# Optimization experiments

Hardware: AMD Instinct MI355X
Metric: run time of the kernel (lower is better)

## Reference

```python
import jax, jax.numpy as jnp
import numpy as np

PRE_NMS_TOP_N = 1024
POST_NMS_TOP_N = 256
NMS_THRESH = 0.7
MIN_SIZE = 4.0
SCORE_THRESH = 0.1
BASE_SIZE = 1024.0
SCALE = 0.25            # feature stride = 1/SCALE = 4
IMG_H, IMG_W = 1024.0, 1024.0
NEG_INF = -1e30
CAP = 8                 # max vertices of 4-gon intersect 4-gon


def setup_inputs() -> dict:
    key = jax.random.key(0)
    k1, k2 = jax.random.split(key)
    N, A, H, W = 2, 1, 256, 256
    objectness = jax.random.normal(k1, (N, A, H, W), dtype=jnp.float32)
    box_regression = jax.random.uniform(k2, (N, A * 5, H, W), dtype=jnp.float32) * 0.05
    return {"objectness": objectness, "box_regression": box_regression}


def eastbox2rbox(reg, H, W):
    # reg: (H*W, 5) -> rotated boxes (H*W, 5) in xywha (angle in degrees)
    jy, jx = jnp.meshgrid(jnp.arange(H, dtype=reg.dtype), jnp.arange(W, dtype=reg.dtype), indexing="ij")
    cx0 = (jx / SCALE).reshape(-1)
    cy0 = (jy / SCALE).reshape(-1)
    t = reg[:, 0] * BASE_SIZE
    r = reg[:, 1] * BASE_SIZE
    b = reg[:, 2] * BASE_SIZE
    l = reg[:, 3] * BASE_SIZE
    ang = (reg[:, 4] - 0.5) * 90.0
    w = l + r
    h = t + b
    xc = cx0 + 0.5 * (r - l)
    yc = cy0 + 0.5 * (b - t)
    return jnp.stack([xc, yc, w, h, ang], axis=-1)


def rbox_corners(box):
    # box: (5,) xywha -> (4,2) CCW corners
    th = box[4] * (jnp.pi / 180.0)
    c, s = jnp.cos(th), jnp.sin(th)
    dx = jnp.array([-0.5, 0.5, 0.5, -0.5], box.dtype) * box[2]
    dy = jnp.array([-0.5, -0.5, 0.5, 0.5], box.dtype) * box[3]
    return jnp.stack([box[0] + dx * c - dy * s, box[1] + dx * s + dy * c], axis=-1)


def clip_halfplane(poly, n, p1, p2):
    # Sutherland-Hodgman clip of a convex polygon (CAP,2) with n valid verts
    # against the half-plane left of directed edge p1->p2.
    M = poly.shape[0]
    idx = jnp.arange(M)
    valid = idx < n
    nxt = poly[jnp.where(idx + 1 < n, idx + 1, 0)]
    e = p2 - p1
    d_cur = e[0] * (poly[:, 1] - p1[1]) - e[1] * (poly[:, 0] - p1[0])
    d_nxt = e[0] * (nxt[:, 1] - p1[1]) - e[1] * (nxt[:, 0] - p1[0])
    in_cur = d_cur >= 0.0
    in_nxt = d_nxt >= 0.0
    denom = d_cur - d_nxt
    safe = jnp.where(jnp.abs(denom) > 1e-9, denom, 1.0)
    t = d_cur / safe
    inter = poly + t[:, None] * (nxt - poly)
    emit_cur = in_cur & valid
    emit_int = (in_cur != in_nxt) & valid
    pts = jnp.stack([poly, inter], axis=1).reshape(2 * M, 2)
    flags = jnp.stack([emit_cur, emit_int], axis=1).reshape(2 * M)
    pos = jnp.where(flags, jnp.cumsum(flags) - 1, M)  # M = dropped
    out = jnp.zeros((M, 2), poly.dtype).at[pos].set(jnp.where(flags[:, None], pts, 0.0), mode="drop")
    return out, jnp.sum(flags)


def intersect_area(pa, pb):
    # area of convex intersection of two 4-gons (each (4,2), CCW)
    poly = jnp.zeros((CAP, 2), pa.dtype).at[:4].set(pa)
    n = jnp.asarray(4, jnp.int32)
    for k in range(4):
        poly, n = clip_halfplane(poly, n, pb[k], pb[(k + 1) % 4])
    idx = jnp.arange(CAP)
    valid = idx < n
    nxt = poly[jnp.where(idx + 1 < n, idx + 1, 0)]
    cr = poly[:, 0] * nxt[:, 1] - nxt[:, 0] * poly[:, 1]
    area = 0.5 * jnp.abs(jnp.sum(jnp.where(valid, cr, 0.0)))
    return jnp.where(n >= 3, area, 0.0)


def riou(a, b):
    inter = intersect_area(rbox_corners(a), rbox_corners(b))
    union = a[2] * a[3] + b[2] * b[3] - inter
    return inter / jnp.maximum(union, 1e-9)


def greedy_nms(iou_mat, valid, thresh):
    K = valid.shape[0]
    ar = jnp.arange(K)

    def body(i, state):
        keep, sup = state
        is_keep = valid[i] & jnp.logical_not(sup[i])
        keep = keep.at[i].set(is_keep)
        sup = sup | (is_keep & (iou_mat[i] > thresh) & (ar > i))
        return keep, sup

    keep, _ = jax.lax.fori_loop(0, K, body, (jnp.zeros(K, bool), jnp.zeros(K, bool)))
    return keep


def process_image(obj, reg):
    A, H, W = obj.shape
    scores = obj.transpose(1, 2, 0).reshape(-1)       # (H*W*A,)
    reg5 = reg[:5].transpose(1, 2, 0).reshape(-1, 5)  # (H*W, 5)
    rboxes = eastbox2rbox(reg5, H, W)
    top_scores, top_idx = jax.lax.top_k(scores, PRE_NMS_TOP_N)
    boxes = rboxes[top_idx]
    valid = top_scores > SCORE_THRESH                 # eval-mode score thresh (masked, not dropped)
    # clip_to_image: clamp rotated-box centers into the image
    boxes = boxes.at[:, 0].set(jnp.clip(boxes[:, 0], 0.0, IMG_W - 1.0))
    boxes = boxes.at[:, 1].set(jnp.clip(boxes[:, 1], 0.0, IMG_H - 1.0))
    # remove_small_boxes
    valid = valid & (boxes[:, 2] >= MIN_SIZE) & (boxes[:, 3] >= MIN_SIZE)
    # full rotated IoU matrix, row-by-row to bound memory
    iou_mat = jax.lax.map(lambda a: jax.vmap(lambda b: riou(a, b))(boxes), boxes)
    keep = greedy_nms(iou_mat, valid, NMS_THRESH)
    sel = jnp.where(keep, top_scores, NEG_INF)
    fin_scores, fin_idx = jax.lax.top_k(sel, POST_NMS_TOP_N)
    fin_boxes = boxes[fin_idx]
    fin_valid = keep[fin_idx]
    out = jnp.concatenate([fin_boxes, fin_scores[:, None]], axis=-1)  # (post, 6) = xywha + score
    return jnp.where(fin_valid[:, None], out, 0.0)


def reference(objectness, box_regression):
    return jax.vmap(process_image)(objectness, box_regression)
```

## Files before the change

### kernel.cpp

```cpp
#include <hip/hip_runtime.h>
#include <hip/hip_bf16.h>

#define N_IMG 2
#define HW 65536
#define PRE 1024
#define POST 256
#define NBIN 4096
#define SORTN 4096
#define NMS_THR 0.7f
#define SCORE_T 0.1f
#define MIN_SZ 4.0f
#define TRIPAIRS 523776
#define TRITOTAL (2 * TRIPAIRS)

__device__ __forceinline__ unsigned int fkey(float f) {
    unsigned int u = __float_as_uint(f);
    return u ^ ((u & 0x80000000u) ? 0xFFFFFFFFu : 0x80000000u);
}
__device__ __forceinline__ float unfkey(unsigned int k) {
    unsigned int u = (k & 0x80000000u) ? (k ^ 0x80000000u) : ~k;
    return __uint_as_float(u);
}
__device__ __forceinline__ unsigned long long readlane64(unsigned long long v, int l) {
    unsigned int lo = (unsigned int)__builtin_amdgcn_readlane((int)(unsigned int)v, l);
    unsigned int hi = (unsigned int)__builtin_amdgcn_readlane((int)(unsigned int)(v >> 32), l);
    return ((unsigned long long)hi << 32) | (unsigned long long)lo;
}

__global__ __launch_bounds__(1024) void k_front(const float* __restrict__ obj,
                                                unsigned int* phist,
                                                unsigned long long* masks,
                                                unsigned int* cnts) {
    __shared__ unsigned int lh[NBIN];
    int img = blockIdx.x >> 3;
    int seg = blockIdx.x & 7;
    for (int i = threadIdx.x; i < NBIN; i += 1024) lh[i] = 0u;
    {
        unsigned long long* mz = masks + (size_t)blockIdx.x * 2048;
        mz[threadIdx.x] = 0ULL;
        mz[threadIdx.x + 1024] = 0ULL;
    }
    if (blockIdx.x == 0 && threadIdx.x < 8) cnts[threadIdx.x] = 0u;
    __syncthreads();
    const float4* o4 = (const float4*)(obj + (size_t)img * HW);
    int base = seg * 2048;
#pragma unroll
    for (int k = 0; k < 2; ++k) {
        float4 v = o4[base + threadIdx.x + k * 1024];
        atomicAdd(&lh[fkey(v.x) >> 20], 1u);
        atomicAdd(&lh[fkey(v.y) >> 20], 1u);
        atomicAdd(&lh[fkey(v.z) >> 20], 1u);
        atomicAdd(&lh[fkey(v.w) >> 20], 1u);
    }
    __syncthreads();
    unsigned int* ph = phist + (size_t)blockIdx.x * NBIN;
    for (int i = threadIdx.x; i < NBIN; i += 1024) ph[i] = lh[i];
}

__global__ void k_findbin(const unsigned int* __restrict__ phist, unsigned int* selB) {
    __shared__ unsigned int lh[NBIN];
    __shared__ unsigned int chunk[256];
    int img = blockIdx.x;
    int t = threadIdx.x;
    for (int c = 0; c < 16; ++c) {
        int b = c * 256 + t;
        unsigned int v = 0;
#pragma unroll
        for (int q = 0; q < 8; ++q) v += phist[(size_t)(img * 8 + q) * NBIN + b];
        lh[b] = v;
    }
    __syncthreads();
    unsigned int s = 0;
    for (int k = 0; k < 16; ++k) s += lh[t * 16 + k];
    chunk[t] = s;
    __syncthreads();
    if (t == 0) {
        unsigned int run = 0;
        int c;
        for (c = 255; c >= 0; --c) {
            if (run + chunk[c] >= PRE) break;
            run += chunk[c];
        }
        unsigned int B = 0;
        for (int b = c * 16 + 15; b >= c * 16; --b) {
            if (run + lh[b] >= PRE) { B = (unsigned int)b; break; }
            run += lh[b];
        }
        selB[img] = B;
    }
}

__global__ __launch_bounds__(256) void k_compact(const float* __restrict__ obj,
                                                 const unsigned int* __restrict__ selB,
                                                 unsigned int* cnts, unsigned long long* cbuf) {
    __shared__ unsigned long long lbuf[1024];
    __shared__ unsigned int lcnt, lbase;
    int t = blockIdx.x * 256 + threadIdx.x;
    const float4* o4 = (const float4*)obj;
#pragma unroll
    for (int k = 0; k < 2; ++k) {
        if (threadIdx.x == 0) lcnt = 0;
        __syncthreads();
        int p = t + k * 16384;
        int img = p >> 14;
        unsigned int B = selB[img];
        float4 v = o4[p];
        float vs[4] = {v.x, v.y, v.z, v.w};
#pragma unroll
        for (int c = 0; c < 4; ++c) {
            unsigned int key = fkey(vs[c]);
            if ((key >> 20) >= B) {
                unsigned int i = (unsigned int)((p & 16383) * 4 + c);
                unsigned int pos = atomicAdd(&lcnt, 1u);
                lbuf[pos] = ((unsigned long long)key << 32) |
                            (unsigned long long)(0xFFFFFFFFu - i);
            }
        }
        __syncthreads();
        if (threadIdx.x == 0) lbase = atomicAdd(&cnts[img], lcnt);
        __syncthreads();
        unsigned int n = lcnt, base = lbase;
        for (unsigned int q = threadIdx.x; q < n; q += 256) {
            unsigned int gp = base + q;
            if (gp < SORTN) cbuf[img * SORTN + gp] = lbuf[q];
        }
        __syncthreads();
    }
}

__device__ __forceinline__ void decode_one(unsigned long long cv, int img,
                                           const float* __restrict__ boxreg,
                                           float* boxes, float* corn, float4* circ,
                                           unsigned int* varr, float* tscr, int r) {
    int g = img * PRE + r;
    unsigned int key = (unsigned int)(cv >> 32);
    unsigned int idx = (0xFFFFFFFFu - (unsigned int)(cv & 0xFFFFFFFFULL)) & 0xFFFFu;
    float sc = unfkey(key);
    int h = (int)(idx >> 8);
    int w = (int)(idx & 255u);
    const float* rg = boxreg + (size_t)img * 5 * HW;
    float t_ = rg[0 * HW + idx] * 1024.0f;
    float rr = rg[1 * HW + idx] * 1024.0f;
    float bb = rg[2 * HW + idx] * 1024.0f;
    float ll = rg[3 * HW + idx] * 1024.0f;
    float ang = (rg[4 * HW + idx] - 0.5f) * 90.0f;
    float wd = ll + rr;
    float ht = t_ + bb;
    float xc = (float)w * 4.0f + 0.5f * (rr - ll);
    float yc = (float)h * 4.0f + 0.5f * (bb - t_);
    xc = fminf(fmaxf(xc, 0.0f), 1023.0f);
    yc = fminf(fmaxf(yc, 0.0f), 1023.0f);
    bool valid = (sc > SCORE_T) && (wd >= MIN_SZ) && (ht >= MIN_SZ);

    float* bx = boxes + (size_t)g * 5;
    bx[0] = xc; bx[1] = yc; bx[2] = wd; bx[3] = ht; bx[4] = ang;
    tscr[g] = sc;
    varr[g] = valid ? 1u : 0u;

    float th = ang * (float)(3.14159265358979323846 / 180.0);
    float c = cosf(th), s = sinf(th);
    const float dxs[4] = {-0.5f, 0.5f, 0.5f, -0.5f};
    const float dys[4] = {-0.5f, -0.5f, 0.5f, 0.5f};
    float* cr = corn + (size_t)g * 8;
#pragma unroll
    for (int k = 0; k < 4; ++k) {
        float dx = dxs[k] * wd, dy = dys[k] * ht;
        cr[2 * k]     = xc + dx * c - dy * s;
        cr[2 * k + 1] = yc + dx * s + dy * c;
    }
    circ[g] = make_float4(xc, yc, 0.5f * sqrtf(wd * wd + ht * ht) + 0.01f, wd * ht);
}

__global__ __launch_bounds__(256) void k_rankdec(const unsigned int* __restrict__ cnts,
                                                 const unsigned long long* __restrict__ cbuf,
                                                 const float* __restrict__ boxreg,
                                                 float* boxes, float* corn, float4* circ,
                                                 unsigned int* varr, float* tscr) {
    __shared__ unsigned long long keys[SORTN];
    int img = blockIdx.x >> 4;
    int slice = blockIdx.x & 15;
    unsigned int M = cnts[img]; if (M > SORTN) M = SORTN;
    for (unsigned int i = threadIdx.x; i < M; i += 256) keys[i] = cbuf[img * SORTN + i];
    __syncthreads();
    unsigned int cid = (unsigned int)slice * 256 + threadIdx.x;
    if (cid >= M) return;
    unsigned long long cv = keys[cid];
    unsigned int r = 0;
    for (unsigned int j = 0; j < M; ++j) r += (keys[j] > cv) ? 1u : 0u;
    if (r < PRE) decode_one(cv, img, boxreg, boxes, corn, circ, varr, tscr, (int)r);
}

__global__ __launch_bounds__(256) void k_pairclip(const float4* __restrict__ circ,
                                                  const float* __restrict__ corn,
                                                  unsigned long long* masks) {
    __shared__ struct {
        float SPX[8][256], SPY[8][256], SQX[8][256], SQY[8][256];
        unsigned int plist[1280];
    } e;
    __shared__ unsigned int pcnt;
    int tid = threadIdx.x;
    if (tid == 0) pcnt = 0;
    __syncthreads();
    int t0 = blockIdx.x * 256 + tid;
    for (int k = 0; k < 8; ++k) {
        int s = t0 + k * 131072;
        if (s < TRITOTAL) {
            int img = (s >= TRIPAIRS) ? 1 : 0;
            int p = s - img * TRIPAIRS;
            int r = (int)((sqrtf((float)(8 * p + 1)) - 1.0f) * 0.5f);
            while ((r * (r + 1)) / 2 > p) --r;
            while (((r + 1) * (r + 2)) / 2 <= p) ++r;
            int i = p - (r * (r + 1)) / 2;
            int j = r + 1;
            float4 a = circ[img * PRE + i];
            float4 b = circ[img * PRE + j];
            float dx = b.x - a.x, dy = b.y - a.y, rr = a.z + b.z;
            if (dx * dx + dy * dy <= rr * rr)
                e.plist[atomicAdd(&pcnt, 1u)] =
                    ((unsigned int)img << 20) | ((unsigned int)i << 10) | (unsigned int)j;
        }
        __syncthreads();
        unsigned int n = pcnt;
        if (n >= 1024 || k == 7) {
            for (unsigned int q = tid; q < n; q += 256) {
                unsigned int pr = e.plist[q];
                int im = (int)(pr >> 20);
                int bi = (int)((pr >> 10) & 1023);
                int bj = (int)(pr & 1023);
                int ra = im * PRE + bi, rb = im * PRE + bj;
                const float4* ca = (const float4*)(corn + (size_t)ra * 8);
                float4 a0 = ca[0], a1 = ca[1];
                const float4* cb = (const float4*)(corn + (size_t)rb * 8);
                float4 b0 = cb[0], b1 = cb[1];
                float cbx[4] = {b0.x, b0.z, b1.x, b1.z};
                float cby[4] = {b0.y, b0.w, b1.y, b1.w};
                e.SPX[0][tid] = a0.x; e.SPY[0][tid] = a0.y;
                e.SPX[1][tid] = a0.z; e.SPY[1][tid] = a0.w;
                e.SPX[2][tid] = a1.x; e.SPY[2][tid] = a1.y;
                e.SPX[3][tid] = a1.z; e.SPY[3][tid] = a1.w;
                int n2 = 4;
#pragma unroll
                for (int ed = 0; ed < 4; ++ed) {
                    float (*PX)[256] = (ed & 1) ? e.SQX : e.SPX;
                    float (*PY)[256] = (ed & 1) ? e.SQY : e.SPY;
                    float (*QX)[256] = (ed & 1) ? e.SPX : e.SQX;
                    float (*QY)[256] = (ed & 1) ? e.SPY : e.SQY;
                    float p1x = cbx[ed], p1y = cby[ed];
                    int e2 = (ed + 1) & 3;
                    float ex = cbx[e2] - p1x, ey = cby[e2] - p1y;
                    int m = 0;
                    for (int kk = 0; kk < n2; ++kk) {
                        int kn = (kk + 1 < n2) ? kk + 1 : 0;
                        float cx_ = PX[kk][tid], cy_ = PY[kk][tid];
                        float nx_ = PX[kn][tid], ny_ = PY[kn][tid];
                        float dc = ex * (cy_ - p1y) - ey * (cx_ - p1x);
                        float dn = ex * (ny_ - p1y) - ey * (nx_ - p1x);
                        bool ic = dc >= 0.0f;
                        bool inx = dn >= 0.0f;
                        if (ic && m < 8) { QX[m][tid] = cx_; QY[m][tid] = cy_; ++m; }
                        if ((ic != inx) && m < 8) {
                            float den = dc - dn;
                            float safe = (fabsf(den) > 1e-9f) ? den : 1.0f;
                            float tt = dc / safe;
                            QX[m][tid] = cx_ + tt * (nx_ - cx_);
                            QY[m][tid] = cy_ + tt * (ny_ - cy_);
                            ++m;
                        }
                    }
                    n2 = m;
                }
                float inter = 0.0f;
                if (n2 >= 3) {
                    float sa = 0.0f;
                    for (int kk = 0; kk < n2; ++kk) {
                        int kn = (kk + 1 < n2) ? kk + 1 : 0;
                        sa += e.SPX[kk][tid] * e.SPY[kn][tid] - e.SPX[kn][tid] * e.SPY[kk][tid];
                    }
                    inter = 0.5f * fabsf(sa);
                }
                float uni = circ[ra].w + circ[rb].w - inter;
                float iou = inter / fmaxf(uni, 1e-9f);
                if (iou > NMS_THR)
                    atomicOr(&masks[(size_t)ra * 16 + (bj >> 6)], 1ULL << (bj & 63));
            }
            __syncthreads();
            if (tid == 0) pcnt = 0;
            __syncthreads();
        }
    }
}

__global__ __launch_bounds__(1024) void k_nms_out(const unsigned long long* __restrict__ masks,
                                                  const unsigned int* __restrict__ varr,
                                                  const float* __restrict__ boxes,
                                                  const float* __restrict__ tscr,
                                                  float* __restrict__ out) {
    __shared__ unsigned long long lm[PRE * 16];
    __shared__ unsigned long long vmw_s[16];
    __shared__ unsigned short keptIdx[POST];
    __shared__ int sTotal;
    int img = blockIdx.x;
    int t = threadIdx.x;
    const unsigned long long* mbase = masks + (size_t)img * PRE * 16;
    {
        const ulonglong2* src = (const ulonglong2*)mbase;
        ulonglong2* dst = (ulonglong2*)lm;
#pragma unroll
        for (int k = 0; k < 8; ++k) dst[t + k * 1024] = src[t + k * 1024];
    }
    {
        unsigned long long bal = __ballot(varr[img * PRE + t] != 0u);
        if ((t & 63) == 0) vmw_s[t >> 6] = bal;
    }
    __syncthreads();
    if (t < 64) {
        int lane = t;
        int lw = lane & 15;
        unsigned long long vmw = vmw_s[lw];
        unsigned long long supw = 0ULL;
        int cnt = 0;
        for (int b = 0; b < 16 && cnt < POST; ++b) {
            unsigned long long avail = readlane64(vmw, b) & ~readlane64(supw, b);
            while (avail && cnt < POST) {
                unsigned long long a = avail;
                int d0 = __ffsll((long long)a) - 1; a &= a - 1;
                int d1 = a ? __ffsll((long long)a) - 1 : 64; a &= a - 1;
                int d2 = a ? __ffsll((long long)a) - 1 : 64; a &= a - 1;
                int d3 = a ? __ffsll((long long)a) - 1 : 64; a &= a - 1;
                int d4 = a ? __ffsll((long long)a) - 1 : 64; a &= a - 1;
                int d5 = a ? __ffsll((long long)a) - 1 : 64; a &= a - 1;
                int d6 = a ? __ffsll((long long)a) - 1 : 64; a &= a - 1;
                int d7 = a ? __ffsll((long long)a) - 1 : 64; a &= a - 1;
                int r0 = b * 64 + d0;
                int r1 = b * 64 + (d1 & 63);
                int r2 = b * 64 + (d2 & 63);
                int r3 = b * 64 + (d3 & 63);
                int r4 = b * 64 + (d4 & 63);
                int r5 = b * 64 + (d5 & 63);
                int r6 = b * 64 + (d6 & 63);
                int r7 = b * 64 + (d7 & 63);
                unsigned long long w0 = lm[r0 * 16 + lw];
                unsigned long long w1 = lm[r1 * 16 + lw];
                unsigned long long w2 = lm[r2 * 16 + lw];
                unsigned long long w3 = lm[r3 * 16 + lw];
                unsigned long long w4 = lm[r4 * 16 + lw];
                unsigned long long w5 = lm[r5 * 16 + lw];
                unsigned long long w6 = lm[r6 * 16 + lw];
                unsigned long long w7 = lm[r7 * 16 + lw];
                unsigned long long sb = readlane64(w0, b);
                supw |= w0;
                if (lane == 0) keptIdx[cnt] = (unsigned short)r0;
                ++cnt;
                if (d1 < 64 && cnt < POST && !((sb >> d1) & 1ULL)) {
                    sb |= readlane64(w1, b); supw |= w1;
                    if (lane == 0) keptIdx[cnt] = (unsigned short)r1;
                    ++cnt;
                }
                if (d2 < 64 && cnt < POST && !((sb >> d2) & 1ULL)) {
                    sb |= readlane64(w2, b); supw |= w2;
                    if (lane == 0) keptIdx[cnt] = (unsigned short)r2;
                    ++cnt;
                }
                if (d3 < 64 && cnt < POST && !((sb >> d3) & 1ULL)) {
                    sb |= readlane64(w3, b); supw |= w3;
                    if (lane == 0) keptIdx[cnt] = (unsigned short)r3;
                    ++cnt;
                }
                if (d4 < 64 && cnt < POST && !((sb >> d4) & 1ULL)) {
                    sb |= readlane64(w4, b); supw |= w4;
                    if (lane == 0) keptIdx[cnt] = (unsigned short)r4;
                    ++cnt;
                }
                if (d5 < 64 && cnt < POST && !((sb >> d5) & 1ULL)) {
                    sb |= readlane64(w5, b); supw |= w5;
                    if (lane == 0) keptIdx[cnt] = (unsigned short)r5;
                    ++cnt;
                }
                if (d6 < 64 && cnt < POST && !((sb >> d6) & 1ULL)) {
                    sb |= readlane64(w6, b); supw |= w6;
                    if (lane == 0) keptIdx[cnt] = (unsigned short)r6;
                    ++cnt;
                }
                if (d7 < 64 && cnt < POST && !((sb >> d7) & 1ULL)) {
                    sb |= readlane64(w7, b); supw |= w7;
                    if (lane == 0) keptIdx[cnt] = (unsigned short)r7;
                    ++cnt;
                }
                avail = a & ~sb;
            }
        }
        if (lane == 0) sTotal = cnt;
    }
    __syncthreads();
    int total = sTotal;
    if (t < POST) {
        float v0 = 0.f, v1 = 0.f, v2 = 0.f, v3 = 0.f, v4 = 0.f, v5 = 0.f;
        if (t < total) {
            int i = keptIdx[t];
            const float* b = boxes + (size_t)(img * PRE + i) * 5;
            v0 = b[0]; v1 = b[1]; v2 = b[2]; v3 = b[3]; v4 = b[4];
            v5 = tscr[img * PRE + i];
        }
        float* o2 = out + (size_t)(img * POST + t) * 6;
        o2[0] = v0; o2[1] = v1; o2[2] = v2; o2[3] = v3; o2[4] = v4; o2[5] = v5;
    }
}

enum : size_t {
    OFF_BOX   = 0,
    OFF_CORN  = 40960,
    OFF_CIRC  = 106496,
    OFF_VARR  = 139264,
    OFF_TSCR  = 147456,
    OFF_MASK  = 155648,
    OFF_PHIST = 417792,
    OFF_CNTS  = 679936,
    OFF_SELB  = 679968,
    OFF_CBUF  = 679984,
};

extern "C" void kernel_launch(void* const* d_in, const int* in_sizes, int n_in,
                              void* d_out, int out_size, void* d_ws, size_t ws_size,
                              hipStream_t stream) {
    const float* obj = (const float*)d_in[0];
    const float* boxreg = (const float*)d_in[1];
    float* out = (float*)d_out;

    char* w = (char*)d_ws;
    float* boxes = (float*)(w + OFF_BOX);
    float* corn = (float*)(w + OFF_CORN);
    float4* circ = (float4*)(w + OFF_CIRC);
    unsigned int* varr = (unsigned int*)(w + OFF_VARR);
    float* tscr = (float*)(w + OFF_TSCR);
    unsigned long long* masks = (unsigned long long*)(w + OFF_MASK);
    unsigned int* phist = (unsigned int*)(w + OFF_PHIST);
    unsigned int* cnts = (unsigned int*)(w + OFF_CNTS);
    unsigned int* selB = (unsigned int*)(w + OFF_SELB);
    unsigned long long* cbuf = (unsigned long long*)(w + OFF_CBUF);

    k_front<<<16, 1024, 0, stream>>>(obj, phist, masks, cnts);
    k_findbin<<<N_IMG, 256, 0, stream>>>(phist, selB);
    k_compact<<<64, 256, 0, stream>>>(obj, selB, cnts, cbuf);
    k_rankdec<<<32, 256, 0, stream>>>(cnts, cbuf, boxreg, boxes, corn, circ, varr, tscr);
    k_pairclip<<<512, 256, 0, stream>>>(circ, corn, masks);
    k_nms_out<<<N_IMG, 1024, 0, stream>>>(masks, varr, boxes, tscr, out);
}
```

Before: 83.44 us.

## Fuse threshold-bin search into compact kernel and split histogram into two copies

Removes the separate k_findbin launch. Each of the 64 compact blocks now redundantly reduces the 8 partial histograms per image and finds the top-k threshold bin in shared memory before compacting, which saves one kernel launch and the global selB round trip. In exchange every block re-reads 2×8×4096 histogram entries and runs a serial scan on one thread. The front kernel also splits the shared histogram into two copies by half-block to reduce atomic contention, then sums the copies on writeout.

```diff
diff --git a/kernel.cpp b/kernel.cpp
--- a/kernel.cpp
+++ b/kernel.cpp
@@ -31,10 +31,11 @@
                                                 unsigned int* phist,
                                                 unsigned long long* masks,
                                                 unsigned int* cnts) {
-    __shared__ unsigned int lh[NBIN];
+    __shared__ unsigned int lh[2][NBIN];
     int img = blockIdx.x >> 3;
     int seg = blockIdx.x & 7;
-    for (int i = threadIdx.x; i < NBIN; i += 1024) lh[i] = 0u;
+    int cp = (threadIdx.x >> 9) & 1;
+    for (int i = threadIdx.x; i < NBIN; i += 1024) { lh[0][i] = 0u; lh[1][i] = 0u; }
     {
         unsigned long long* mz = masks + (size_t)blockIdx.x * 2048;
         mz[threadIdx.x] = 0ULL;
@@ -47,63 +48,65 @@
 #pragma unroll
     for (int k = 0; k < 2; ++k) {
         float4 v = o4[base + threadIdx.x + k * 1024];
-        atomicAdd(&lh[fkey(v.x) >> 20], 1u);
-        atomicAdd(&lh[fkey(v.y) >> 20], 1u);
-        atomicAdd(&lh[fkey(v.z) >> 20], 1u);
-        atomicAdd(&lh[fkey(v.w) >> 20], 1u);
+        atomicAdd(&lh[cp][fkey(v.x) >> 20], 1u);
+        atomicAdd(&lh[cp][fkey(v.y) >> 20], 1u);
+        atomicAdd(&lh[cp][fkey(v.z) >> 20], 1u);
+        atomicAdd(&lh[cp][fkey(v.w) >> 20], 1u);
     }
     __syncthreads();
     unsigned int* ph = phist + (size_t)blockIdx.x * NBIN;
-    for (int i = threadIdx.x; i < NBIN; i += 1024) ph[i] = lh[i];
-}
-
-__global__ void k_findbin(const unsigned int* __restrict__ phist, unsigned int* selB) {
+    for (int i = threadIdx.x; i < NBIN; i += 1024) ph[i] = lh[0][i] + lh[1][i];
+}
+
+__global__ __launch_bounds__(256) void k_compact(const float* __restrict__ obj,
+                                                 const unsigned int* __restrict__ phist,
+                                                 unsigned int* cnts, unsigned long long* cbuf) {
     __shared__ unsigned int lh[NBIN];
     __shared__ unsigned int chunk[256];
-    int img = blockIdx.x;
-    int t = threadIdx.x;
-    for (int c = 0; c < 16; ++c) {
-        int b = c * 256 + t;
-        unsigned int v = 0;
-#pragma unroll
-        for (int q = 0; q < 8; ++q) v += phist[(size_t)(img * 8 + q) * NBIN + b];
-        lh[b] = v;
-    }
-    __syncthreads();
-    unsigned int s = 0;
-    for (int k = 0; k < 16; ++k) s += lh[t * 16 + k];
-    chunk[t] = s;
-    __syncthreads();
-    if (t == 0) {
-        unsigned int run = 0;
-        int c;
-        for (c = 255; c >= 0; --c) {
-            if (run + chunk[c] >= PRE) break;
-            run += chunk[c];
-        }
-        unsigned int B = 0;
-        for (int b = c * 16 + 15; b >= c * 16; --b) {
-            if (run + lh[b] >= PRE) { B = (unsigned int)b; break; }
-            run += lh[b];
-        }
-        selB[img] = B;
-    }
-}
-
-__global__ __launch_bounds__(256) void k_compact(const float* __restrict__ obj,
-                                                 const unsigned int* __restrict__ selB,
-                                                 unsigned int* cnts, unsigned long long* cbuf) {
+    __shared__ unsigned int sB[2];
     __shared__ unsigned long long lbuf[1024];
     __shared__ unsigned int lcnt, lbase;
-    int t = blockIdx.x * 256 + threadIdx.x;
+    int tid = threadIdx.x;
+
+    for (int img = 0; img < N_IMG; ++img) {
+        for (int c = 0; c < 16; ++c) {
+            int b = c * 256 + tid;
+            unsigned int v = 0;
+#pragma unroll
+            for (int q = 0; q < 8; ++q) v += phist[(size_t)(img * 8 + q) * NBIN + b];
+            lh[b] = v;
+        }
+        __syncthreads();
+        unsigned int s = 0;
+        for (int k = 0; k < 16; ++k) s += lh[tid * 16 + k];
+        chunk[tid] = s;
+        __syncthreads();
+        if (tid == 0) {
+            unsigned int run = 0;
+            int c;
+            for (c = 255; c >= 0; --c) {
+                if (run + chunk[c] >= PRE) break;
+                run += chunk[c];
+            }
+            unsigned int B = 0;
+            for (int b = c * 16 + 15; b >= c * 16; --b) {
+                if (run + lh[b] >= PRE) { B = (unsigned int)b; break; }
+                run += lh[b];
+            }
+            sB[img] = B;
+        }
+        __syncthreads();
+    }
+
+    int t = blockIdx.x * 256 + tid;
     const float4* o4 = (const float4*)obj;
 #pragma unroll
-    for (int k = 0; k < 2; ++k) {
-        if (threadIdx.x == 0) lcnt = 0;
+    for (int k = 0; k < N_IMG; ++k) {
+        if (tid == 0) lcnt = 0;
         __syncthreads();
         int p = t + k * 16384;
         int img = p >> 14;
-        unsigned int B = selB[img];
+        unsigned int B = sB[img];
         float4 v = o4[p];
         float vs[4] = {v.x, v.y, v.z, v.w};
 #pragma unroll
@@ -117,10 +120,10 @@
             }
         }
         __syncthreads();
-        if (threadIdx.x == 0) lbase = atomicAdd(&cnts[img], lcnt);
+        if (tid == 0) lbase = atomicAdd(&cnts[img], lcnt);
         __syncthreads();
         unsigned int n = lcnt, base = lbase;
-        for (unsigned int q = threadIdx.x; q < n; q += 256) {
+        for (unsigned int q = tid; q < n; q += 256) {
             unsigned int gp = base + q;
             if (gp < SORTN) cbuf[img * SORTN + gp] = lbuf[q];
         }
@@ -415,8 +418,7 @@
     OFF_MASK  = 155648,
     OFF_PHIST = 417792,
     OFF_CNTS  = 679936,
-    OFF_SELB  = 679968,
-    OFF_CBUF  = 679984,
+    OFF_CBUF  = 679968,
 };
 
 extern "C" void kernel_launch(void* const* d_in, const int* in_sizes, int n_in,
@@ -435,12 +437,10 @@
     unsigned long long* masks = (unsigned long long*)(w + OFF_MASK);
     unsigned int* phist = (unsigned int*)(w + OFF_PHIST);
     unsigned int* cnts = (unsigned int*)(w + OFF_CNTS);
-    unsigned int* selB = (unsigned int*)(w + OFF_SELB);
     unsigned long long* cbuf = (unsigned long long*)(w + OFF_CBUF);
 
     k_front<<<16, 1024, 0, stream>>>(obj, phist, masks, cnts);
-    k_findbin<<<N_IMG, 256, 0, stream>>>(phist, selB);
-    k_compact<<<64, 256, 0, stream>>>(obj, selB, cnts, cbuf);
+    k_compact<<<64, 256, 0, stream>>>(obj, phist, cnts, cbuf);
     k_rankdec<<<32, 256, 0, stream>>>(cnts, cbuf, boxreg, boxes, corn, circ, varr, tscr);
     k_pairclip<<<512, 256, 0, stream>>>(circ, corn, masks);
     k_nms_out<<<N_IMG, 1024, 0, stream>>>(masks, varr, boxes, tscr, out);
```

After: 86.40 us. +3.5%, slower.
